# Kernel tuning notes

Hardware: AMD Instinct MI355X
Metric: run time of the kernel (lower is better)

Reference implementation:

```python
import jax, jax.numpy as jnp
import numpy as np

N = 100000   # num nodes
E = 600000   # num edges
H = 128      # hidden dim
R = 8        # num relations
B = 4        # num bases


def setup_inputs() -> dict:
    key = jax.random.key(0)
    ks = jax.random.split(key, 12)
    return {
        "node_ids": jnp.arange(N, dtype=jnp.int64 if jax.config.jax_enable_x64 else jnp.int32),
        "src": jax.random.randint(ks[0], (E,), 0, N),
        "dst": jax.random.randint(ks[1], (E,), 0, N),
        "etype": jax.random.randint(ks[2], (E,), 0, R),
        "embedding": jax.random.normal(ks[3], (N, H), dtype=jnp.float32),
        "V1": jax.random.normal(ks[4], (B, H, H), dtype=jnp.float32) * 0.05,
        "comp1": jax.random.normal(ks[5], (R, B), dtype=jnp.float32),
        "loop1": jax.random.normal(ks[6], (H, H), dtype=jnp.float32) * 0.05,
        "bias1": jax.random.normal(ks[7], (H,), dtype=jnp.float32) * 0.05,
        "V2": jax.random.normal(ks[8], (B, H, H), dtype=jnp.float32) * 0.05,
        "comp2": jax.random.normal(ks[9], (R, B), dtype=jnp.float32),
        "loop2": jax.random.normal(ks[10], (H, H), dtype=jnp.float32) * 0.05,
        "bias2": jax.random.normal(ks[11], (H,), dtype=jnp.float32) * 0.05,
    }


def _rgcn_layer(h, src, dst, etype, V, comp, loopW, bias, activate):
    # basis decomposition: W_r = sum_b comp[r,b] * V[b]   -> [R, in, out]
    W = jnp.einsum('rb,bio->rio', comp, V)
    # transform all nodes under all relations once (avoids per-edge GEMM): [N, R, out]
    hw = jnp.einsum('ni,rio->nro', h, W)
    # gather per-edge message for its (src, relation): [E, out]
    m = hw[src, etype]
    # scatter-sum aggregation at destination nodes
    agg = jax.ops.segment_sum(m, dst, num_segments=h.shape[0])
    out = agg + bias + h @ loopW  # bias + self-loop
    return jax.nn.relu(out) if activate else out


def reference(node_ids, src, dst, etype, embedding,
              V1, comp1, loop1, bias1,
              V2, comp2, loop2, bias2):
    h = embedding[node_ids]                       # EmbeddingLayer
    h = _rgcn_layer(h, src, dst, etype, V1, comp1, loop1, bias1, activate=True)
    h = _rgcn_layer(h, src, dst, etype, V2, comp2, loop2, bias2, activate=False)
    return h
```

## Files before the change

### kernel.cpp

```cpp
#include <hip/hip_runtime.h>
#include <hip/hip_bf16.h>

#define NN 100000
#define NE 600000
#define HH 128
#define NB 4
#define TILE 2048
#define NTILES ((NN + TILE - 1) / TILE)

typedef __attribute__((ext_vector_type(8))) short bf16x8;
typedef __attribute__((ext_vector_type(4))) float f32x4;
typedef __attribute__((ext_vector_type(4))) float vfloat4;
typedef __attribute__((ext_vector_type(4))) unsigned short ushort4v;

static __device__ __forceinline__ short f2bf(float f) {
  unsigned u = __float_as_uint(f);
  unsigned r = (u + 0x7fffu + ((u >> 16) & 1u)) >> 16;
  return (short)r;
}

static __device__ __forceinline__ void build_one(const float* __restrict__ V,
                                                 const float* __restrict__ loopW,
                                                 short* __restrict__ W8, int idx)
{
  int j  = idx & 7;
  int o  = (idx >> 3) & 127;
  int kb = idx >> 10;
  int k  = kb * 8 + j;
  float v;
  if (k < 512) v = V[(size_t)k * HH + o];
  else         v = loopW[(size_t)(k - 512) * HH + o];
  W8[idx] = f2bf(v);
}

__global__ __launch_bounds__(256) void prep_all(
    const float* __restrict__ V1, const float* __restrict__ loop1, short* __restrict__ W81,
    const float* __restrict__ V2, const float* __restrict__ loop2, short* __restrict__ W82,
    const float* __restrict__ emb, short* __restrict__ hbf1,
    const int* __restrict__ dst, int* __restrict__ deg)
{
  const int bid = blockIdx.x;
  if (bid < 320) {
    build_one(V1, loop1, W81, bid * 256 + threadIdx.x);
  } else if (bid < 640) {
    build_one(V2, loop2, W82, (bid - 320) * 256 + threadIdx.x);
  } else if (bid < 2984) {
    int e = (bid - 640) * 256 + threadIdx.x;
    if (e < NE) atomicAdd(&deg[dst[e]], 1);
  } else {
    const int n8 = NN * HH / 8;
    int i = (bid - 2984) * 256 + threadIdx.x;
    for (; i < n8; i += 800 * 256) {
      const vfloat4* p = reinterpret_cast<const vfloat4*>(emb + (size_t)i * 8);
      vfloat4 a = p[0], b = p[1];
      bf16x8 o;
#pragma unroll
      for (int j = 0; j < 4; ++j) { o[j] = f2bf(a[j]); o[j + 4] = f2bf(b[j]); }
      reinterpret_cast<bf16x8*>(hbf1)[i] = o;
    }
  }
}


__global__ __launch_bounds__(256) void scan_tiles(const int* __restrict__ deg,
                                                  int* __restrict__ tilesum)
{
  __shared__ int red[256];
  const int tid = threadIdx.x;
  int base = blockIdx.x * TILE + tid * 8;
  int s = 0;
#pragma unroll
  for (int j = 0; j < 8; ++j) {
    int i = base + j;
    if (i < NN) s += deg[i];
  }
  red[tid] = s;
  __syncthreads();
  for (int off = 128; off > 0; off >>= 1) {
    if (tid < off) red[tid] += red[tid + off];
    __syncthreads();
  }
  if (tid == 0) tilesum[blockIdx.x] = red[0];
}

__global__ __launch_bounds__(256) void scan_final(const int* deg,
                                                  const int* __restrict__ tilesum,
                                                  int* __restrict__ rowptr,
                                                  int* cursor)
{
  __shared__ int lds[256];
  const int tid = threadIdx.x;
  int pre = 0;
  for (int t = 0; t < NTILES; ++t)
    if (t < blockIdx.x) pre += tilesum[t];

  int base = blockIdx.x * TILE + tid * 8;
  int d[8];
  int s = 0;
#pragma unroll
  for (int j = 0; j < 8; ++j) {
    int i = base + j;
    d[j] = (i < NN) ? deg[i] : 0;
    s += d[j];
  }
  lds[tid] = s;
  __syncthreads();
  for (int off = 1; off < 256; off <<= 1) {
    int t = (tid >= off) ? lds[tid - off] : 0;
    __syncthreads();
    lds[tid] += t;
    __syncthreads();
  }
  int run = pre + lds[tid] - s;
#pragma unroll
  for (int j = 0; j < 8; ++j) {
    int i = base + j;
    if (i < NN) {
      rowptr[i] = run;
      cursor[i] = run;
      run += d[j];
    }
  }
  if (blockIdx.x == NTILES - 1 && tid == 255)
    rowptr[NN] = pre + lds[255];
}

__global__ __launch_bounds__(256) void scatter_edges(
    const int* __restrict__ src, const int* __restrict__ dst, const int* __restrict__ ety,
    int* __restrict__ cursor, int* __restrict__ csr)
{
  int e = blockIdx.x * blockDim.x + threadIdx.x;
  if (e >= NE) return;
  int d = dst[e];
  int p = atomicAdd(&cursor[d], 1);
  csr[p] = src[e] | (ety[e] << 20);
}

template<int FINAL>
__global__ __launch_bounds__(512, 6) void rgcn_fused(
    const int* __restrict__ rowptr, const int* __restrict__ csr,
    const float* __restrict__ comp,
    const short* __restrict__ hbf,
    const short* __restrict__ W8,
    const float* __restrict__ bias,
    short* __restrict__ outH,
    float* __restrict__ outF)
{
  __shared__ bf16x8 gl[32][64];
  __shared__ bf16x8 wl[2][512];

  const int tid  = threadIdx.x;
  const int wave = tid >> 6;
  const int lane = tid & 63;
  const int b  = lane >> 4;
  const int q  = lane & 15;
  const int base = blockIdx.x * 32;
  const int l4 = lane * 4;

  const int mt = wave >> 2;
  const int ct0 = (wave & 3) * 2;
  const int mynode = base + mt * 16 + q;

  const bf16x8* wsrc = reinterpret_cast<const bf16x8*>(W8);
  bf16x8 w0reg = wsrc[tid];

  const char* hbytes = reinterpret_cast<const char*>(hbf);
  unsigned* glu = reinterpret_cast<unsigned*>(gl);

  {
    const int r0 = wave * 4;
    int ii[4], EE[4];
    ii[0] = __builtin_amdgcn_readfirstlane(rowptr[base + r0]);
    EE[0] = __builtin_amdgcn_readfirstlane(rowptr[base + r0 + 1]);
    ii[1] = EE[0];
    EE[1] = __builtin_amdgcn_readfirstlane(rowptr[base + r0 + 2]);
    ii[2] = EE[1];
    EE[2] = __builtin_amdgcn_readfirstlane(rowptr[base + r0 + 3]);
    ii[3] = EE[2];
    EE[3] = __builtin_amdgcn_readfirstlane(rowptr[base + r0 + 4]);

    float acc[4][8] = {};

    while (ii[0] < EE[0] || ii[1] < EE[1] || ii[2] < EE[2] || ii[3] < EE[3]) {
      unsigned hq[16];
      int es[16];
#pragma unroll
      for (int n = 0; n < 4; ++n) {
        if (ii[n] < EE[n]) {
#pragma unroll
          for (int j = 0; j < 4; ++j) {
            const int idx = ii[n] + j;
            const int e = __builtin_amdgcn_readfirstlane(
                csr[idx < EE[n] ? idx : EE[n] - 1]);
            es[n * 4 + j] = e;
            hq[n * 4 + j] = *reinterpret_cast<const unsigned*>(
                hbytes + (((size_t)(e & 0xFFFFF)) << 8) + l4);
          }
        }
      }
#pragma unroll
      for (int n = 0; n < 4; ++n) {
        if (ii[n] < EE[n]) {
#pragma unroll
          for (int j = 0; j < 4; ++j) {
            const int idx = ii[n] + j;
            const bool v = idx < EE[n];
            const int e = es[n * 4 + j];
            const float lo = __uint_as_float(hq[n * 4 + j] << 16);
            const float hi = __uint_as_float(hq[n * 4 + j] & 0xffff0000u);
#pragma unroll
            for (int B = 0; B < 4; ++B) {
              const float c = v ? comp[(e >> 20) * NB + B] : 0.f;
              acc[n][2 * B]     += c * lo;
              acc[n][2 * B + 1] += c * hi;
            }
          }
          ii[n] += 4;
        }
      }
    }

#pragma unroll
    for (int n = 0; n < 4; ++n) {
      const int row = r0 + n;
#pragma unroll
      for (int B = 0; B < 4; ++B) {
        unsigned w = ((unsigned)(unsigned short)f2bf(acc[n][2 * B + 1]) << 16) |
                     (unsigned short)f2bf(acc[n][2 * B]);
        const int s = B * 16 + (lane >> 2);
        glu[row * 256 + ((s ^ (row & 7)) << 2) + (lane & 3)] = w;
      }
    }
  }

  const bf16x8* ha = reinterpret_cast<const bf16x8*>(hbf + (size_t)mynode * HH);
  bf16x8 hreg[4];
#pragma unroll
  for (int j = 0; j < 4; ++j) hreg[j] = ha[j * 4 + b];

  wl[0][tid] = w0reg;
  __syncthreads();

  const int r  = q;
  const int g8 = b;

  f32x4 acc0 = {0.f, 0.f, 0.f, 0.f};
  f32x4 acc1 = {0.f, 0.f, 0.f, 0.f};

#pragma unroll 1
  for (int ks = 0; ks < 20; ++ks) {
    const int cur = ks & 1;
    bf16x8 nxt;
    if (ks < 19) nxt = wsrc[(ks + 1) * 512 + tid];
    bf16x8 a = (ks < 16) ? gl[mt * 16 + r][(ks * 4 + g8) ^ (r & 7)] : hreg[ks - 16];
    bf16x8 w0 = wl[cur][g8 * 128 + (ct0 + 0) * 16 + r];
    bf16x8 w1 = wl[cur][g8 * 128 + (ct0 + 1) * 16 + r];
    acc0 = __builtin_amdgcn_mfma_f32_16x16x32_bf16(w0, a, acc0, 0, 0, 0);
    acc1 = __builtin_amdgcn_mfma_f32_16x16x32_bf16(w1, a, acc1, 0, 0, 0);
    if (ks < 19) wl[cur ^ 1][tid] = nxt;
    __syncthreads();
  }

  if (FINAL) {
    float* glf = reinterpret_cast<float*>(gl);
#pragma unroll
    for (int c = 0; c < 2; ++c) {
      const f32x4 acc = c ? acc1 : acc0;
      const int row = mt * 16 + r;
      const int o = (ct0 + c) * 16 + g8 * 4;
      vfloat4 bs = *reinterpret_cast<const vfloat4*>(bias + o);
      vfloat4 x;
#pragma unroll
      for (int rr = 0; rr < 4; ++rr) x[rr] = acc[rr] + bs[rr];
      const int s = (ct0 + c) * 4 + g8;
      const int phys = s ^ (row & 7);
      *reinterpret_cast<vfloat4*>(glf + row * 128 + phys * 4) = x;
    }
    __syncthreads();
#pragma unroll
    for (int p = 0; p < 2; ++p) {
      const int flat = p * 512 + tid;
      const int row = flat >> 5, s = flat & 31;
      const int phys = s ^ (row & 7);
      vfloat4 x = *reinterpret_cast<const vfloat4*>(glf + row * 128 + phys * 4);
      *reinterpret_cast<vfloat4*>(outF + (size_t)(base + row) * HH + s * 4) = x;
    }
  } else {
    short* glb = reinterpret_cast<short*>(gl);
#pragma unroll
    for (int c = 0; c < 2; ++c) {
      const f32x4 acc = c ? acc1 : acc0;
      const int row = mt * 16 + r;
      const int o = (ct0 + c) * 16 + g8 * 4;
      vfloat4 bs = *reinterpret_cast<const vfloat4*>(bias + o);
      ushort4v sv;
#pragma unroll
      for (int rr = 0; rr < 4; ++rr)
        sv[rr] = (unsigned short)f2bf(fmaxf(acc[rr] + bs[rr], 0.f));
      const int u8 = (ct0 + c) * 4 + g8;
      const int phys16 = (u8 >> 1) ^ (row & 7);
      *reinterpret_cast<ushort4v*>(glb + row * 128 + phys16 * 8 + (u8 & 1) * 4) = sv;
    }
    __syncthreads();
    {
      const int row = tid >> 4, s16 = tid & 15;
      const int phys = s16 ^ (row & 7);
      bf16x8 x = *reinterpret_cast<const bf16x8*>(glb + row * 128 + phys * 8);
      *reinterpret_cast<bf16x8*>(outH + (size_t)(base + row) * HH + s16 * 8) = x;
    }
  }
}

extern "C" void kernel_launch(void* const* d_in, const int* in_sizes, int n_in,
                              void* d_out, int out_size, void* d_ws, size_t ws_size,
                              hipStream_t stream)
{
  const int*   srcp  = (const int*)d_in[1];
  const int*   dstp  = (const int*)d_in[2];
  const int*   etp   = (const int*)d_in[3];
  const float* emb   = (const float*)d_in[4];
  const float* V1    = (const float*)d_in[5];
  const float* comp1 = (const float*)d_in[6];
  const float* loop1 = (const float*)d_in[7];
  const float* bias1 = (const float*)d_in[8];
  const float* V2    = (const float*)d_in[9];
  const float* comp2 = (const float*)d_in[10];
  const float* loop2 = (const float*)d_in[11];
  const float* bias2 = (const float*)d_in[12];
  float* out = (float*)d_out;

  char* ws = (char*)d_ws;
  short* Wt1     = (short*)(ws);
  short* Wt2     = (short*)(ws + 163840);
  short* hbf1    = (short*)(ws + 327680);
  short* hbf2    = (short*)(ws + 25927680);
  int*   deg     = (int*)  (ws + 51527680);
  int*   rowptr  = (int*)  (ws + 51927680);
  int*   csr     = (int*)  (ws + 52327696);
  int*   tilesum = (int*)  (ws + 54727696);

  const int fused_blocks = NN / 32;
  const int e_blocks     = (NE + 255) / 256;

  hipMemsetAsync(deg, 0, NN * sizeof(int), stream);

  hipLaunchKernelGGL(prep_all, dim3(3784), dim3(256), 0, stream,
                     V1, loop1, Wt1, V2, loop2, Wt2, emb, hbf1, dstp, deg);

  hipLaunchKernelGGL(scan_tiles, dim3(NTILES), dim3(256), 0, stream, deg, tilesum);
  hipLaunchKernelGGL(scan_final, dim3(NTILES), dim3(256), 0, stream,
                     deg, tilesum, rowptr, deg);
  hipLaunchKernelGGL(scatter_edges, dim3(e_blocks), dim3(256), 0, stream,
                     srcp, dstp, etp, deg, csr);

  hipLaunchKernelGGL((rgcn_fused<0>), dim3(fused_blocks), dim3(512), 0, stream,
                     rowptr, csr, comp1, hbf1, Wt1, bias1, hbf2, (float*)nullptr);

  hipLaunchKernelGGL((rgcn_fused<1>), dim3(fused_blocks), dim3(512), 0, stream,
                     rowptr, csr, comp2, hbf2, Wt2, bias2, (short*)nullptr, out);
}
```

Measured before the change: 289.1 us.

## Merge preprocessing and CSR build into one cooperative kernel with grid syncs

Replaces the memset, prep kernel, two-pass tile scan and edge scatter kernel with a single cooperative kernel of 256 blocks of 1024 threads. Phases are separated by grid-wide barriers, and the scan uses a block-level scan followed by a scan of block sums. This is meant to remove several launch overheads and inter-kernel gaps, at the cost of grid-sync latency and lower occupancy from a fixed 256-block grid during the memory-bound conversion and atomic phases. It relies on 256*1024 covering NN exactly once for the scan.

```diff
diff --git a/kernel.cpp b/kernel.cpp
--- a/kernel.cpp
+++ b/kernel.cpp
@@ -1,12 +1,13 @@
 #include <hip/hip_runtime.h>
 #include <hip/hip_bf16.h>
+#include <hip/hip_cooperative_groups.h>
+
+namespace cg = cooperative_groups;
 
 #define NN 100000
 #define NE 600000
 #define HH 128
 #define NB 4
-#define TILE 2048
-#define NTILES ((NN + TILE - 1) / TILE)
 
 typedef __attribute__((ext_vector_type(8))) short bf16x8;
 typedef __attribute__((ext_vector_type(4))) float f32x4;
@@ -33,107 +34,75 @@
   W8[idx] = f2bf(v);
 }
 
-__global__ __launch_bounds__(256) void prep_all(
+__global__ __launch_bounds__(1024) void coop_build(
     const float* __restrict__ V1, const float* __restrict__ loop1, short* __restrict__ W81,
     const float* __restrict__ V2, const float* __restrict__ loop2, short* __restrict__ W82,
     const float* __restrict__ emb, short* __restrict__ hbf1,
-    const int* __restrict__ dst, int* __restrict__ deg)
+    const int* __restrict__ src, const int* __restrict__ dst, const int* __restrict__ ety,
+    int* __restrict__ deg, int* __restrict__ rowptr, int* __restrict__ csr,
+    int* __restrict__ blocksum)
 {
+  cg::grid_group grid = cg::this_grid();
+  __shared__ int lds[1024];
+  const int tid = threadIdx.x;
   const int bid = blockIdx.x;
-  if (bid < 320) {
-    build_one(V1, loop1, W81, bid * 256 + threadIdx.x);
-  } else if (bid < 640) {
-    build_one(V2, loop2, W82, (bid - 320) * 256 + threadIdx.x);
-  } else if (bid < 2984) {
-    int e = (bid - 640) * 256 + threadIdx.x;
-    if (e < NE) atomicAdd(&deg[dst[e]], 1);
-  } else {
-    const int n8 = NN * HH / 8;
-    int i = (bid - 2984) * 256 + threadIdx.x;
-    for (; i < n8; i += 800 * 256) {
-      const vfloat4* p = reinterpret_cast<const vfloat4*>(emb + (size_t)i * 8);
-      vfloat4 a = p[0], b = p[1];
-      bf16x8 o;
-#pragma unroll
-      for (int j = 0; j < 4; ++j) { o[j] = f2bf(a[j]); o[j + 4] = f2bf(b[j]); }
-      reinterpret_cast<bf16x8*>(hbf1)[i] = o;
-    }
-  }
-}
-
-
-__global__ __launch_bounds__(256) void scan_tiles(const int* __restrict__ deg,
-                                                  int* __restrict__ tilesum)
-{
-  __shared__ int red[256];
-  const int tid = threadIdx.x;
-  int base = blockIdx.x * TILE + tid * 8;
-  int s = 0;
-#pragma unroll
-  for (int j = 0; j < 8; ++j) {
-    int i = base + j;
-    if (i < NN) s += deg[i];
-  }
-  red[tid] = s;
+  const int g = bid * 1024 + tid;
+  const int GT = 256 * 1024;
+
+  for (int i = g; i < NN; i += GT) deg[i] = 0;
+  for (int i = g; i < 81920; i += GT) build_one(V1, loop1, W81, i);
+  for (int i = g; i < 81920; i += GT) build_one(V2, loop2, W82, i);
+  const int n8 = NN * HH / 8;
+  for (int i = g; i < n8; i += GT) {
+    const vfloat4* p = reinterpret_cast<const vfloat4*>(emb + (size_t)i * 8);
+    vfloat4 a = p[0], b = p[1];
+    bf16x8 o;
+#pragma unroll
+    for (int j = 0; j < 4; ++j) { o[j] = f2bf(a[j]); o[j + 4] = f2bf(b[j]); }
+    reinterpret_cast<bf16x8*>(hbf1)[i] = o;
+  }
+  grid.sync();
+
+  for (int e = g; e < NE; e += GT) atomicAdd(&deg[dst[e]], 1);
+  grid.sync();
+
+  const int d = (g < NN) ? deg[g] : 0;
+  lds[tid] = d;
   __syncthreads();
-  for (int off = 128; off > 0; off >>= 1) {
-    if (tid < off) red[tid] += red[tid + off];
-    __syncthreads();
-  }
-  if (tid == 0) tilesum[blockIdx.x] = red[0];
-}
-
-__global__ __launch_bounds__(256) void scan_final(const int* deg,
-                                                  const int* __restrict__ tilesum,
-                                                  int* __restrict__ rowptr,
-                                                  int* cursor)
-{
-  __shared__ int lds[256];
-  const int tid = threadIdx.x;
-  int pre = 0;
-  for (int t = 0; t < NTILES; ++t)
-    if (t < blockIdx.x) pre += tilesum[t];
-
-  int base = blockIdx.x * TILE + tid * 8;
-  int d[8];
-  int s = 0;
-#pragma unroll
-  for (int j = 0; j < 8; ++j) {
-    int i = base + j;
-    d[j] = (i < NN) ? deg[i] : 0;
-    s += d[j];
-  }
-  lds[tid] = s;
+  for (int off = 1; off < 1024; off <<= 1) {
+    int t = (tid >= off) ? lds[tid - off] : 0;
+    __syncthreads();
+    lds[tid] += t;
+    __syncthreads();
+  }
+  const int myexcl = lds[tid] - d;
+  if (tid == 1023) blocksum[bid] = lds[1023];
+  grid.sync();
+
+  if (tid < 256) lds[tid] = blocksum[tid];
   __syncthreads();
   for (int off = 1; off < 256; off <<= 1) {
-    int t = (tid >= off) ? lds[tid - off] : 0;
-    __syncthreads();
-    lds[tid] += t;
-    __syncthreads();
-  }
-  int run = pre + lds[tid] - s;
-#pragma unroll
-  for (int j = 0; j < 8; ++j) {
-    int i = base + j;
-    if (i < NN) {
-      rowptr[i] = run;
-      cursor[i] = run;
-      run += d[j];
-    }
-  }
-  if (blockIdx.x == NTILES - 1 && tid == 255)
-    rowptr[NN] = pre + lds[255];
-}
-
-__global__ __launch_bounds__(256) void scatter_edges(
-    const int* __restrict__ src, const int* __restrict__ dst, const int* __restrict__ ety,
-    int* __restrict__ cursor, int* __restrict__ csr)
-{
-  int e = blockIdx.x * blockDim.x + threadIdx.x;
-  if (e >= NE) return;
-  int d = dst[e];
-  int p = atomicAdd(&cursor[d], 1);
-  csr[p] = src[e] | (ety[e] << 20);
+    int t = 0;
+    if (tid < 256 && tid >= off) t = lds[tid - off];
+    __syncthreads();
+    if (tid < 256) lds[tid] += t;
+    __syncthreads();
+  }
+  const int preBlock = lds[bid] - blocksum[bid];
+  const int run = preBlock + myexcl;
+  if (g < NN) {
+    rowptr[g] = run;
+    deg[g] = run;
+  } else if (g == NN) {
+    rowptr[NN] = run;
+  }
+  grid.sync();
+
+  for (int e = g; e < NE; e += GT) {
+    int dd = dst[e];
+    int p = atomicAdd(&deg[dd], 1);
+    csr[p] = src[e] | (ety[e] << 20);
+  }
 }
 
 template<int FINAL>
@@ -330,28 +299,26 @@
   float* out = (float*)d_out;
 
   char* ws = (char*)d_ws;
-  short* Wt1     = (short*)(ws);
-  short* Wt2     = (short*)(ws + 163840);
-  short* hbf1    = (short*)(ws + 327680);
-  short* hbf2    = (short*)(ws + 25927680);
-  int*   deg     = (int*)  (ws + 51527680);
-  int*   rowptr  = (int*)  (ws + 51927680);
-  int*   csr     = (int*)  (ws + 52327696);
-  int*   tilesum = (int*)  (ws + 54727696);
+  short* Wt1      = (short*)(ws);
+  short* Wt2      = (short*)(ws + 163840);
+  short* hbf1     = (short*)(ws + 327680);
+  short* hbf2     = (short*)(ws + 25927680);
+  int*   deg      = (int*)  (ws + 51527680);
+  int*   rowptr   = (int*)  (ws + 51927680);
+  int*   csr      = (int*)  (ws + 52327696);
+  int*   blocksum = (int*)  (ws + 54727696);
 
   const int fused_blocks = NN / 32;
-  const int e_blocks     = (NE + 255) / 256;
-
-  hipMemsetAsync(deg, 0, NN * sizeof(int), stream);
-
-  hipLaunchKernelGGL(prep_all, dim3(3784), dim3(256), 0, stream,
-                     V1, loop1, Wt1, V2, loop2, Wt2, emb, hbf1, dstp, deg);
-
-  hipLaunchKernelGGL(scan_tiles, dim3(NTILES), dim3(256), 0, stream, deg, tilesum);
-  hipLaunchKernelGGL(scan_final, dim3(NTILES), dim3(256), 0, stream,
-                     deg, tilesum, rowptr, deg);
-  hipLaunchKernelGGL(scatter_edges, dim3(e_blocks), dim3(256), 0, stream,
-                     srcp, dstp, etp, deg, csr);
+
+  void* cargs[] = {
+    (void*)&V1, (void*)&loop1, (void*)&Wt1,
+    (void*)&V2, (void*)&loop2, (void*)&Wt2,
+    (void*)&emb, (void*)&hbf1,
+    (void*)&srcp, (void*)&dstp, (void*)&etp,
+    (void*)&deg, (void*)&rowptr, (void*)&csr, (void*)&blocksum
+  };
+  hipLaunchCooperativeKernel((void*)coop_build, dim3(256), dim3(1024),
+                             cargs, 0, stream);
 
   hipLaunchKernelGGL((rgcn_fused<0>), dim3(fused_blocks), dim3(512), 0, stream,
                      rowptr, csr, comp1, hbf1, Wt1, bias1, hbf2, (float*)nullptr);
```

Result: slower. 404.1 us (+39.8%).
